# Kernel optimization log

Hardware: AMD Instinct MI355X
Metric: run time of the kernel (lower is better)

The kernel has to match this reference:

```python
import jax, jax.numpy as jnp
import numpy as np

B, N, U = 4096, 128, 128  # batch, num_notes, num_units
F = N - 1                 # per-note feature dim; +1 condition scalar -> LSTM input = N
W_SCALE = 0.08            # ~1/sqrt(U), keeps gates in a sane range


def setup_inputs() -> dict:
    key = jax.random.key(0)
    ks = jax.random.split(key, 12)
    return {
        "note_features": jax.random.normal(ks[0], (B, N, F), jnp.float32),
        "targets": jax.random.uniform(ks[1], (B, N), jnp.float32),
        "w_ih0": jax.random.normal(ks[2], (4 * U, N), jnp.float32) * W_SCALE,
        "w_hh0": jax.random.normal(ks[3], (4 * U, U), jnp.float32) * W_SCALE,
        "b_ih0": jax.random.normal(ks[4], (4 * U,), jnp.float32) * W_SCALE,
        "b_hh0": jax.random.normal(ks[5], (4 * U,), jnp.float32) * W_SCALE,
        "w_ih1": jax.random.normal(ks[6], (4 * U, U), jnp.float32) * W_SCALE,
        "w_hh1": jax.random.normal(ks[7], (4 * U, U), jnp.float32) * W_SCALE,
        "b_ih1": jax.random.normal(ks[8], (4 * U,), jnp.float32) * W_SCALE,
        "b_hh1": jax.random.normal(ks[9], (4 * U,), jnp.float32) * W_SCALE,
        "w_out": jax.random.normal(ks[10], (1, U), jnp.float32) * W_SCALE,
        "b_out": jax.random.normal(ks[11], (1,), jnp.float32) * W_SCALE,
    }


def _lstm_cell(x, h, c, w_ih, w_hh, b_ih, b_hh):
    # PyTorch gate order: i, f, g, o
    gates = x @ w_ih.T + b_ih + h @ w_hh.T + b_hh  # [B, 4U]
    i, f, g, o = jnp.split(gates, 4, axis=-1)
    c_new = jax.nn.sigmoid(f) * c + jax.nn.sigmoid(i) * jnp.tanh(g)
    h_new = jax.nn.sigmoid(o) * jnp.tanh(c_new)
    return h_new, c_new


def reference(note_features, targets, w_ih0, w_hh0, b_ih0, b_hh0,
              w_ih1, w_hh1, b_ih1, b_hh1, w_out, b_out):
    b = note_features.shape[0]
    # teacher-forced condition: previous target note, zero at step 0
    cond = jnp.concatenate([jnp.zeros((b, 1), note_features.dtype), targets[:, :-1]], axis=1)
    x_seq = jnp.concatenate([note_features, cond[..., None]], axis=-1)  # [B, N, N]
    x_seq = jnp.transpose(x_seq, (1, 0, 2))                              # [N, B, N]

    zeros = jnp.zeros((b, U), note_features.dtype)

    def step(carry, x):
        h0, c0, h1, c1 = carry
        h0, c0 = _lstm_cell(x, h0, c0, w_ih0, w_hh0, b_ih0, b_hh0)
        h1, c1 = _lstm_cell(h0, h1, c1, w_ih1, w_hh1, b_ih1, b_hh1)
        return (h0, c0, h1, c1), h1

    _, hs = jax.lax.scan(step, (zeros, zeros, zeros, zeros), x_seq)  # [N, B, U]
    logits = jnp.einsum('nbu,ou->nbo', hs, w_out) + b_out            # [N, B, 1]
    return jnp.transpose(jax.nn.sigmoid(logits)[..., 0], (1, 0))     # [B, N]
```

## Files before the change

kernel.cpp:

```cpp
#include <hip/hip_runtime.h>
#include <math.h>

typedef _Float16 f16;
typedef _Float16 f16x8 __attribute__((ext_vector_type(8)));
typedef float f32x4 __attribute__((ext_vector_type(4)));

#define NSTEP 128
#define FEAT  127
#define BLK_B 16
#define NBLOCK 256
#define NTHREADS 512

__device__ __forceinline__ float sigf(float x) { return 1.0f / (1.0f + __expf(-x)); }
__device__ __forceinline__ float tanh_(float x) { return 1.0f - 2.0f / (1.0f + __expf(2.0f * x)); }

__device__ __forceinline__ void sync_lds() {
    asm volatile("s_waitcnt lgkmcnt(0)" ::: "memory");
    __builtin_amdgcn_s_barrier();
    asm volatile("" ::: "memory");
}

#define PIN(v) asm volatile("" : "+v"(v))

__global__ void prep_weights(const float* __restrict__ w_ih0,
                             const float* __restrict__ w_hh0,
                             const float* __restrict__ w_ih1,
                             const float* __restrict__ w_hh1,
                             f16* __restrict__ ws16)
{
    int idx = blockIdx.x * blockDim.x + threadIdx.x;
    int j    = idx & 7;
    int lane = (idx >> 3) & 63;
    int ks   = (idx >> 9) & 3;
    int gate = (idx >> 11) & 3;
    int wave = (idx >> 13) & 7;
    int sel  = (idx >> 16) & 3;
    int n = gate * 128 + wave * 16 + (lane & 15);
    int k = ks * 32 + (lane >> 4) * 8 + j;
    const float* W = (sel == 0) ? w_ih0 : (sel == 1) ? w_hh0 : (sel == 2) ? w_ih1 : w_hh1;
    ws16[idx] = (f16)W[n * 128 + k];
}

__global__ __launch_bounds__(NTHREADS, 2) void lstm_l0(
    const float* __restrict__ nf,   const float* __restrict__ tgt,
    const float* __restrict__ b_ih0, const float* __restrict__ b_hh0,
    const f16* __restrict__ wfrag,  f16* __restrict__ h0g)
{
    __shared__ __align__(16) f16 xs[2][16][152];
    __shared__ __align__(16) f16 h0s[2][16][152];

    const int tid  = threadIdx.x;
    const int wave = tid >> 6;
    const int lane = tid & 63;
    const int col  = lane & 15;
    const int quad = lane >> 4;
    const int b0   = blockIdx.x * BLK_B;
    const int u    = wave * 16 + col;

    for (int i = tid; i < 2 * 16 * 152; i += NTHREADS)
        (&h0s[0][0][0])[i] = (f16)0.0f;

    float bias0[4];
#pragma unroll
    for (int g = 0; g < 4; ++g)
        bias0[g] = b_ih0[g * 128 + u] + b_hh0[g * 128 + u];

    const f16x8* wf = (const f16x8*)wfrag;

    f16x8 wih0[4][4], whh0[4][4];
#pragma unroll
    for (int g = 0; g < 4; ++g)
#pragma unroll
        for (int ks = 0; ks < 4; ++ks) {
            const int fi = ((wave * 4 + g) * 4 + ks) * 64 + lane;
            wih0[g][ks] = wf[0 * 8192 + fi];
            whh0[g][ks] = wf[1 * 8192 + fi];
            PIN(wih0[g][ks]);
            PIN(whh0[g][ks]);
        }

    const float* px[2][2];
    int pxs[2][2];
#pragma unroll
    for (int rr = 0; rr < 2; ++rr) {
        const long rowg = b0 + wave * 2 + rr;
#pragma unroll
        for (int h = 0; h < 2; ++h) {
            const int k = lane + 64 * h;
            if (k < FEAT) { px[rr][h] = nf + (rowg * NSTEP + 1) * FEAT + k; pxs[rr][h] = FEAT; }
            else          { px[rr][h] = tgt + rowg * NSTEP;                 pxs[rr][h] = 1; }
        }
    }

    f16* hp = h0g + (long)(b0 + quad * 4) * NSTEP * 128 + u;

    f32x4 c0 = {0.f, 0.f, 0.f, 0.f};

#pragma unroll
    for (int rr = 0; rr < 2; ++rr) {
        const int row = wave * 2 + rr;
        const long gbt = (long)(b0 + row) * NSTEP;
#pragma unroll
        for (int h = 0; h < 2; ++h) {
            const int k = lane + 64 * h;
            xs[0][row][k] = (f16)((k < FEAT) ? nf[gbt * FEAT + k] : 0.0f);
        }
    }
    sync_lds();

    for (int t = 0; t < NSTEP; ++t) {
        const int pa = t & 1, wb = pa ^ 1;

        float xnv[2][2] = {{0.f, 0.f}, {0.f, 0.f}};
        if (t + 1 < NSTEP) {
#pragma unroll
            for (int rr = 0; rr < 2; ++rr)
#pragma unroll
                for (int h = 0; h < 2; ++h)
                    xnv[rr][h] = *px[rr][h];
        }

        f16x8 ax[4], ah[4];
#pragma unroll
        for (int ks = 0; ks < 4; ++ks) {
            ax[ks] = *(const f16x8*)&xs[pa][col][ks * 32 + quad * 8];
            ah[ks] = *(const f16x8*)&h0s[pa][col][ks * 32 + quad * 8];
        }

        f32x4 accx[4], acch[4];
#pragma unroll
        for (int g = 0; g < 4; ++g) {
            accx[g] = (f32x4){bias0[g], bias0[g], bias0[g], bias0[g]};
            acch[g] = (f32x4){0.f, 0.f, 0.f, 0.f};
        }
#pragma unroll
        for (int ks = 0; ks < 4; ++ks)
#pragma unroll
            for (int g = 0; g < 4; ++g)
                accx[g] = __builtin_amdgcn_mfma_f32_16x16x32_f16(ax[ks], wih0[g][ks], accx[g], 0, 0, 0);
#pragma unroll
        for (int ks = 0; ks < 4; ++ks)
#pragma unroll
            for (int g = 0; g < 4; ++g)
                acch[g] = __builtin_amdgcn_mfma_f32_16x16x32_f16(ah[ks], whh0[g][ks], acch[g], 0, 0, 0);

        float h0n[4];
#pragma unroll
        for (int r = 0; r < 4; ++r) {
            const float ig = sigf(accx[0][r] + acch[0][r]);
            const float fg = sigf(accx[1][r] + acch[1][r]);
            const float gg = tanh_(accx[2][r] + acch[2][r]);
            const float og = sigf(accx[3][r] + acch[3][r]);
            const float cn = fg * c0[r] + ig * gg;
            c0[r] = cn;
            h0n[r] = og * tanh_(cn);
        }
#pragma unroll
        for (int r = 0; r < 4; ++r) {
            h0s[wb][quad * 4 + r][u] = (f16)h0n[r];
            hp[r * (NSTEP * 128)] = (f16)h0n[r];
        }
        hp += 128;

        if (t + 1 < NSTEP) {
#pragma unroll
            for (int rr = 0; rr < 2; ++rr)
#pragma unroll
                for (int h = 0; h < 2; ++h) {
                    xs[wb][wave * 2 + rr][lane + 64 * h] = (f16)xnv[rr][h];
                    px[rr][h] += pxs[rr][h];
                }
        }
        sync_lds();
    }
}

__global__ __launch_bounds__(NTHREADS, 2) void lstm_l1(
    const f16* __restrict__ h0g,
    const float* __restrict__ b_ih1, const float* __restrict__ b_hh1,
    const float* __restrict__ w_out, const float* __restrict__ b_out,
    const f16* __restrict__ wfrag,  float* __restrict__ out)
{
    __shared__ __align__(16) f16 hx[2][16][152];
    __shared__ __align__(16) f16 h1s[2][16][152];
    __shared__ float outp[2][8][16];

    const int tid  = threadIdx.x;
    const int wave = tid >> 6;
    const int lane = tid & 63;
    const int col  = lane & 15;
    const int quad = lane >> 4;
    const int b0   = blockIdx.x * BLK_B;
    const int u    = wave * 16 + col;

    for (int i = tid; i < 2 * 16 * 152; i += NTHREADS)
        (&h1s[0][0][0])[i] = (f16)0.0f;

    float bias1[4];
#pragma unroll
    for (int g = 0; g < 4; ++g)
        bias1[g] = b_ih1[g * 128 + u] + b_hh1[g * 128 + u];
    const float wo_u = w_out[u];
    const float bout = b_out[0];

    const f16x8* wf = (const f16x8*)wfrag;

    f16x8 wih1[4][4], whh1[4][4];
#pragma unroll
    for (int g = 0; g < 4; ++g)
#pragma unroll
        for (int ks = 0; ks < 4; ++ks) {
            const int fi = ((wave * 4 + g) * 4 + ks) * 64 + lane;
            wih1[g][ks] = wf[2 * 8192 + fi];
            whh1[g][ks] = wf[3 * 8192 + fi];
            PIN(wih1[g][ks]);
            PIN(whh1[g][ks]);
        }

    const unsigned* rp[2];
#pragma unroll
    for (int rr = 0; rr < 2; ++rr) {
        const int row = wave * 2 + rr;
        rp[rr] = (const unsigned*)(h0g + ((long)(b0 + row) * NSTEP + 1) * 128) + lane;
    }

    f32x4 c1 = {0.f, 0.f, 0.f, 0.f};

#pragma unroll
    for (int rr = 0; rr < 2; ++rr) {
        const int row = wave * 2 + rr;
        const unsigned* sp = (const unsigned*)(h0g + ((long)(b0 + row) * NSTEP) * 128);
        *(unsigned*)&hx[0][row][lane * 2] = sp[lane];
    }
    sync_lds();

    for (int t = 0; t < NSTEP; ++t) {
        const int pa = t & 1, wb = pa ^ 1;

        unsigned hnv[2] = {0u, 0u};
        if (t + 1 < NSTEP) {
#pragma unroll
            for (int rr = 0; rr < 2; ++rr)
                hnv[rr] = rp[rr][0];
        }

        f16x8 axv[4], ahv[4];
#pragma unroll
        for (int ks = 0; ks < 4; ++ks) {
            axv[ks] = *(const f16x8*)&hx[pa][col][ks * 32 + quad * 8];
            ahv[ks] = *(const f16x8*)&h1s[pa][col][ks * 32 + quad * 8];
        }

        f32x4 accx[4], acch[4];
#pragma unroll
        for (int g = 0; g < 4; ++g) {
            accx[g] = (f32x4){bias1[g], bias1[g], bias1[g], bias1[g]};
            acch[g] = (f32x4){0.f, 0.f, 0.f, 0.f};
        }
#pragma unroll
        for (int ks = 0; ks < 4; ++ks)
#pragma unroll
            for (int g = 0; g < 4; ++g)
                accx[g] = __builtin_amdgcn_mfma_f32_16x16x32_f16(axv[ks], wih1[g][ks], accx[g], 0, 0, 0);
#pragma unroll
        for (int ks = 0; ks < 4; ++ks)
#pragma unroll
            for (int g = 0; g < 4; ++g)
                acch[g] = __builtin_amdgcn_mfma_f32_16x16x32_f16(ahv[ks], whh1[g][ks], acch[g], 0, 0, 0);

        float h1n[4];
#pragma unroll
        for (int r = 0; r < 4; ++r) {
            const float ig = sigf(accx[0][r] + acch[0][r]);
            const float fg = sigf(accx[1][r] + acch[1][r]);
            const float gg = tanh_(accx[2][r] + acch[2][r]);
            const float og = sigf(accx[3][r] + acch[3][r]);
            const float cn = fg * c1[r] + ig * gg;
            c1[r] = cn;
            h1n[r] = og * tanh_(cn);
        }
#pragma unroll
        for (int r = 0; r < 4; ++r)
            h1s[wb][quad * 4 + r][u] = (f16)h1n[r];

        float ps[4];
#pragma unroll
        for (int r = 0; r < 4; ++r) ps[r] = h1n[r] * wo_u;
#pragma unroll
        for (int m = 1; m < 16; m <<= 1) {
#pragma unroll
            for (int r = 0; r < 4; ++r) ps[r] += __shfl_xor(ps[r], m, 64);
        }
        if (col == 0) {
#pragma unroll
            for (int r = 0; r < 4; ++r) outp[pa][wave][quad * 4 + r] = ps[r];
        }

        if (t + 1 < NSTEP) {
#pragma unroll
            for (int rr = 0; rr < 2; ++rr) {
                *(unsigned*)&hx[wb][wave * 2 + rr][lane * 2] = hnv[rr];
                rp[rr] += 64;
            }
        }

        sync_lds();

        if (tid < 16) {
            float s = bout;
#pragma unroll
            for (int w = 0; w < 8; ++w) s += outp[pa][w][tid];
            out[(long)(b0 + tid) * NSTEP + t] = sigf(s);
        }
    }
}

__global__ __launch_bounds__(NTHREADS, 2) void lstm_fb(
    const float* __restrict__ nf,   const float* __restrict__ tgt,
    const float* __restrict__ b_ih0, const float* __restrict__ b_hh0,
    const float* __restrict__ b_ih1, const float* __restrict__ b_hh1,
    const float* __restrict__ w_out, const float* __restrict__ b_out,
    const f16* __restrict__ wfrag,  float* __restrict__ out)
{
    __shared__ f16 xs[2][16][152];
    __shared__ f16 h0s[2][16][152];
    __shared__ f16 h1s[2][16][152];
    __shared__ float outp[8][16];

    const int tid  = threadIdx.x;
    const int wave = tid >> 6;
    const int lane = tid & 63;
    const int col  = lane & 15;
    const int quad = lane >> 4;
    const int b0   = blockIdx.x * BLK_B;
    const int u    = wave * 16 + col;

    for (int i = tid; i < 2 * 16 * 152; i += NTHREADS) {
        (&h0s[0][0][0])[i] = (f16)0.0f;
        (&h1s[0][0][0])[i] = (f16)0.0f;
    }
    float bias0[4], bias1[4];
#pragma unroll
    for (int g = 0; g < 4; ++g) {
        bias0[g] = b_ih0[g * 128 + u] + b_hh0[g * 128 + u];
        bias1[g] = b_ih1[g * 128 + u] + b_hh1[g * 128 + u];
    }
    const float wo_u = w_out[u];
    const float bout = b_out[0];
    const f16x8* wf = (const f16x8*)wfrag;

    f32x4 c0 = {0.f, 0.f, 0.f, 0.f};
    f32x4 c1 = {0.f, 0.f, 0.f, 0.f};

#pragma unroll
    for (int rr = 0; rr < 2; ++rr) {
        const int row = wave * 2 + rr;
        const long gbt = (long)(b0 + row) * NSTEP;
#pragma unroll
        for (int h = 0; h < 2; ++h) {
            const int k = lane + 64 * h;
            xs[0][row][k] = (f16)((k < FEAT) ? nf[gbt * FEAT + k] : 0.0f);
        }
    }
    __syncthreads();

    for (int t = 0; t < NSTEP; ++t) {
        const int pa = t & 1, wb = pa ^ 1;
        float xnv[2][2];
#pragma unroll
        for (int rr = 0; rr < 2; ++rr) {
            const int row = wave * 2 + rr;
#pragma unroll
            for (int h = 0; h < 2; ++h) {
                const int k = lane + 64 * h;
                float v = 0.0f;
                if (t + 1 < NSTEP) {
                    const long gbt = (long)(b0 + row) * NSTEP + (t + 1);
                    v = (k < FEAT) ? nf[gbt * FEAT + k] : tgt[(long)(b0 + row) * NSTEP + t];
                }
                xnv[rr][h] = v;
            }
        }
        f32x4 acc[4];
#pragma unroll
        for (int g = 0; g < 4; ++g) acc[g] = (f32x4){bias0[g], bias0[g], bias0[g], bias0[g]};
#pragma unroll
        for (int ks = 0; ks < 4; ++ks) {
            f16x8 a = *(const f16x8*)&xs[pa][col][ks * 32 + quad * 8];
#pragma unroll
            for (int g = 0; g < 4; ++g) {
                f16x8 b = wf[((wave * 4 + g) * 4 + ks) * 64 + lane];
                acc[g] = __builtin_amdgcn_mfma_f32_16x16x32_f16(a, b, acc[g], 0, 0, 0);
            }
        }
#pragma unroll
        for (int ks = 0; ks < 4; ++ks) {
            f16x8 a = *(const f16x8*)&h0s[pa][col][ks * 32 + quad * 8];
#pragma unroll
            for (int g = 0; g < 4; ++g) {
                f16x8 b = wf[1 * 8192 + ((wave * 4 + g) * 4 + ks) * 64 + lane];
                acc[g] = __builtin_amdgcn_mfma_f32_16x16x32_f16(a, b, acc[g], 0, 0, 0);
            }
        }
        float h0n[4];
#pragma unroll
        for (int r = 0; r < 4; ++r) {
            const float ig = sigf(acc[0][r]);
            const float fg = sigf(acc[1][r]);
            const float gg = tanh_(acc[2][r]);
            const float og = sigf(acc[3][r]);
            const float cn = fg * c0[r] + ig * gg;
            c0[r] = cn;
            h0n[r] = og * tanh_(cn);
        }
#pragma unroll
        for (int r = 0; r < 4; ++r) h0s[wb][quad * 4 + r][u] = (f16)h0n[r];
        __syncthreads();

#pragma unroll
        for (int g = 0; g < 4; ++g) acc[g] = (f32x4){bias1[g], bias1[g], bias1[g], bias1[g]};
#pragma unroll
        for (int ks = 0; ks < 4; ++ks) {
            f16x8 a = *(const f16x8*)&h0s[wb][col][ks * 32 + quad * 8];
#pragma unroll
            for (int g = 0; g < 4; ++g) {
                f16x8 b = wf[2 * 8192 + ((wave * 4 + g) * 4 + ks) * 64 + lane];
                acc[g] = __builtin_amdgcn_mfma_f32_16x16x32_f16(a, b, acc[g], 0, 0, 0);
            }
        }
#pragma unroll
        for (int ks = 0; ks < 4; ++ks) {
            f16x8 a = *(const f16x8*)&h1s[pa][col][ks * 32 + quad * 8];
#pragma unroll
            for (int g = 0; g < 4; ++g) {
                f16x8 b = wf[3 * 8192 + ((wave * 4 + g) * 4 + ks) * 64 + lane];
                acc[g] = __builtin_amdgcn_mfma_f32_16x16x32_f16(a, b, acc[g], 0, 0, 0);
            }
        }
        float h1n[4];
#pragma unroll
        for (int r = 0; r < 4; ++r) {
            const float ig = sigf(acc[0][r]);
            const float fg = sigf(acc[1][r]);
            const float gg = tanh_(acc[2][r]);
            const float og = sigf(acc[3][r]);
            const float cn = fg * c1[r] + ig * gg;
            c1[r] = cn;
            h1n[r] = og * tanh_(cn);
        }
#pragma unroll
        for (int r = 0; r < 4; ++r) h1s[wb][quad * 4 + r][u] = (f16)h1n[r];
#pragma unroll
        for (int rr = 0; rr < 2; ++rr) {
            const int row = wave * 2 + rr;
#pragma unroll
            for (int h = 0; h < 2; ++h) xs[wb][row][lane + 64 * h] = (f16)xnv[rr][h];
        }
        float ps[4];
#pragma unroll
        for (int r = 0; r < 4; ++r) ps[r] = h1n[r] * wo_u;
#pragma unroll
        for (int m = 1; m < 16; m <<= 1) {
#pragma unroll
            for (int r = 0; r < 4; ++r) ps[r] += __shfl_xor(ps[r], m, 64);
        }
        if (col == 0) {
#pragma unroll
            for (int r = 0; r < 4; ++r) outp[wave][quad * 4 + r] = ps[r];
        }
        __syncthreads();
        if (tid < 16) {
            float s = bout;
#pragma unroll
            for (int w = 0; w < 8; ++w) s += outp[w][tid];
            out[(long)(b0 + tid) * NSTEP + t] = sigf(s);
        }
    }
}

extern "C" void kernel_launch(void* const* d_in, const int* in_sizes, int n_in,
                              void* d_out, int out_size, void* d_ws, size_t ws_size,
                              hipStream_t stream)
{
    const float* nf    = (const float*)d_in[0];
    const float* tgt   = (const float*)d_in[1];
    const float* w_ih0 = (const float*)d_in[2];
    const float* w_hh0 = (const float*)d_in[3];
    const float* b_ih0 = (const float*)d_in[4];
    const float* b_hh0 = (const float*)d_in[5];
    const float* w_ih1 = (const float*)d_in[6];
    const float* w_hh1 = (const float*)d_in[7];
    const float* b_ih1 = (const float*)d_in[8];
    const float* b_hh1 = (const float*)d_in[9];
    const float* w_out = (const float*)d_in[10];
    const float* b_out = (const float*)d_in[11];

    f16*   ws16 = (f16*)d_ws;
    float* out  = (float*)d_out;

    prep_weights<<<1024, 256, 0, stream>>>(w_ih0, w_hh0, w_ih1, w_hh1, ws16);

    const size_t need = 512 * 1024 + (size_t)4096 * 128 * 128 * 2;
    if (ws_size >= need) {
        f16* h0g = ws16 + 4 * 65536;
        lstm_l0<<<NBLOCK, NTHREADS, 0, stream>>>(nf, tgt, b_ih0, b_hh0, ws16, h0g);
        lstm_l1<<<NBLOCK, NTHREADS, 0, stream>>>(h0g, b_ih1, b_hh1, w_out, b_out, ws16, out);
    } else {
        lstm_fb<<<NBLOCK, NTHREADS, 0, stream>>>(nf, tgt, b_ih0, b_hh0, b_ih1, b_hh1,
                                                 w_out, b_out, ws16, out);
    }
}
```

Before: 800.2 us.

## Fuse layer-0 and layer-1 LSTM kernels into one launch, drop weight prep

Merges the two per-layer kernels into a single kernel that runs layer 0 over all steps, then layer 1, in the same block. This removes the separate weight-prep launch and two extra launches by converting fp32 weights to f16 fragments directly in registers. Layer 1 now loads its h0 input fragments straight from global memory into registers, prefetched one step ahead, instead of staging them through LDS. The output-projection reduction uses DPP row operations instead of shuffles, and the first MFMA of each gate starts from the bias vector or zero. The cost is strided fp32 weight loads at startup and an h0 round-trip through global memory inside one kernel, which now relies on the block reading back only what it wrote.

```diff
diff --git a/kernel.cpp b/kernel.cpp
--- a/kernel.cpp
+++ b/kernel.cpp
@@ -21,6 +21,263 @@
 }
 
 #define PIN(v) asm volatile("" : "+v"(v))
+
+__device__ __forceinline__ f16x8 load_wfrag(const float* __restrict__ W, int n, int k) {
+    const float* p = W + n * 128 + k;
+    f16x8 r;
+#pragma unroll
+    for (int j = 0; j < 8; ++j) r[j] = (f16)p[j];
+    return r;
+}
+
+__device__ __forceinline__ float row16_sum(float v) {
+    int t;
+    t = __builtin_amdgcn_update_dpp(0, __float_as_int(v), 0x118, 0xf, 0xf, true);
+    v += __int_as_float(t);
+    t = __builtin_amdgcn_update_dpp(0, __float_as_int(v), 0x114, 0xf, 0xf, true);
+    v += __int_as_float(t);
+    t = __builtin_amdgcn_update_dpp(0, __float_as_int(v), 0x112, 0xf, 0xf, true);
+    v += __int_as_float(t);
+    t = __builtin_amdgcn_update_dpp(0, __float_as_int(v), 0x111, 0xf, 0xf, true);
+    v += __int_as_float(t);
+    return v;
+}
+
+__global__ __launch_bounds__(NTHREADS, 2) void lstm_fused(
+    const float* __restrict__ nf,    const float* __restrict__ tgt,
+    const float* __restrict__ w_ih0, const float* __restrict__ w_hh0,
+    const float* __restrict__ b_ih0, const float* __restrict__ b_hh0,
+    const float* __restrict__ w_ih1, const float* __restrict__ w_hh1,
+    const float* __restrict__ b_ih1, const float* __restrict__ b_hh1,
+    const float* __restrict__ w_out, const float* __restrict__ b_out,
+    f16* __restrict__ h0g, float* __restrict__ out)
+{
+    __shared__ __align__(16) f16 bufA[2][16][152];
+    __shared__ __align__(16) f16 bufB[2][16][152];
+    __shared__ float outp[2][8][16];
+
+    const int tid  = threadIdx.x;
+    const int wave = tid >> 6;
+    const int lane = tid & 63;
+    const int col  = lane & 15;
+    const int quad = lane >> 4;
+    const int b0   = blockIdx.x * BLK_B;
+    const int u    = wave * 16 + col;
+    const f32x4 zz = {0.f, 0.f, 0.f, 0.f};
+
+    {
+        for (int i = tid; i < 2 * 16 * 152; i += NTHREADS)
+            (&bufB[0][0][0])[i] = (f16)0.0f;
+
+        f32x4 bv0[4];
+#pragma unroll
+        for (int g = 0; g < 4; ++g) {
+            const float b = b_ih0[g * 128 + u] + b_hh0[g * 128 + u];
+            bv0[g] = (f32x4){b, b, b, b};
+        }
+
+        f16x8 wih0[4][4], whh0[4][4];
+#pragma unroll
+        for (int g = 0; g < 4; ++g)
+#pragma unroll
+            for (int ks = 0; ks < 4; ++ks) {
+                wih0[g][ks] = load_wfrag(w_ih0, g * 128 + u, ks * 32 + quad * 8);
+                whh0[g][ks] = load_wfrag(w_hh0, g * 128 + u, ks * 32 + quad * 8);
+                PIN(wih0[g][ks]);
+                PIN(whh0[g][ks]);
+            }
+
+        const float* px[2][2];
+        int pxs[2][2];
+#pragma unroll
+        for (int rr = 0; rr < 2; ++rr) {
+            const long rowg = b0 + wave * 2 + rr;
+#pragma unroll
+            for (int h = 0; h < 2; ++h) {
+                const int k = lane + 64 * h;
+                if (k < FEAT) { px[rr][h] = nf + (rowg * NSTEP + 1) * FEAT + k; pxs[rr][h] = FEAT; }
+                else          { px[rr][h] = tgt + rowg * NSTEP;                 pxs[rr][h] = 1; }
+            }
+        }
+
+        f16* hp = h0g + (long)(b0 + quad * 4) * NSTEP * 128 + u;
+
+        f32x4 c0 = {0.f, 0.f, 0.f, 0.f};
+
+#pragma unroll
+        for (int rr = 0; rr < 2; ++rr) {
+            const int row = wave * 2 + rr;
+            const long gbt = (long)(b0 + row) * NSTEP;
+#pragma unroll
+            for (int h = 0; h < 2; ++h) {
+                const int k = lane + 64 * h;
+                bufA[0][row][k] = (f16)((k < FEAT) ? nf[gbt * FEAT + k] : 0.0f);
+            }
+        }
+        sync_lds();
+
+        for (int t = 0; t < NSTEP; ++t) {
+            const int pa = t & 1, wb = pa ^ 1;
+
+            float xnv[2][2] = {{0.f, 0.f}, {0.f, 0.f}};
+            if (t + 1 < NSTEP) {
+#pragma unroll
+                for (int rr = 0; rr < 2; ++rr)
+#pragma unroll
+                    for (int h = 0; h < 2; ++h)
+                        xnv[rr][h] = *px[rr][h];
+            }
+
+            f16x8 ax[4], ah[4];
+#pragma unroll
+            for (int ks = 0; ks < 4; ++ks) {
+                ax[ks] = *(const f16x8*)&bufA[pa][col][ks * 32 + quad * 8];
+                ah[ks] = *(const f16x8*)&bufB[pa][col][ks * 32 + quad * 8];
+            }
+
+            f32x4 accx[4], acch[4];
+#pragma unroll
+            for (int g = 0; g < 4; ++g) {
+                accx[g] = __builtin_amdgcn_mfma_f32_16x16x32_f16(ax[0], wih0[g][0], bv0[g], 0, 0, 0);
+                acch[g] = __builtin_amdgcn_mfma_f32_16x16x32_f16(ah[0], whh0[g][0], zz, 0, 0, 0);
+            }
+#pragma unroll
+            for (int ks = 1; ks < 4; ++ks)
+#pragma unroll
+                for (int g = 0; g < 4; ++g) {
+                    accx[g] = __builtin_amdgcn_mfma_f32_16x16x32_f16(ax[ks], wih0[g][ks], accx[g], 0, 0, 0);
+                    acch[g] = __builtin_amdgcn_mfma_f32_16x16x32_f16(ah[ks], whh0[g][ks], acch[g], 0, 0, 0);
+                }
+
+            float h0n[4];
+#pragma unroll
+            for (int r = 0; r < 4; ++r) {
+                const float ig = sigf(accx[0][r] + acch[0][r]);
+                const float fg = sigf(accx[1][r] + acch[1][r]);
+                const float gg = tanh_(accx[2][r] + acch[2][r]);
+                const float og = sigf(accx[3][r] + acch[3][r]);
+                const float cn = fg * c0[r] + ig * gg;
+                c0[r] = cn;
+                h0n[r] = og * tanh_(cn);
+            }
+#pragma unroll
+            for (int r = 0; r < 4; ++r) {
+                bufB[wb][quad * 4 + r][u] = (f16)h0n[r];
+                hp[r * (NSTEP * 128)] = (f16)h0n[r];
+            }
+            hp += 128;
+
+            if (t + 1 < NSTEP) {
+#pragma unroll
+                for (int rr = 0; rr < 2; ++rr)
+#pragma unroll
+                    for (int h = 0; h < 2; ++h) {
+                        bufA[wb][wave * 2 + rr][lane + 64 * h] = (f16)xnv[rr][h];
+                        px[rr][h] += pxs[rr][h];
+                    }
+            }
+            sync_lds();
+        }
+    }
+
+    __syncthreads();
+    for (int i = tid; i < 2 * 16 * 152; i += NTHREADS)
+        (&bufA[0][0][0])[i] = (f16)0.0f;
+    __syncthreads();
+
+    {
+        f32x4 bv1[4];
+#pragma unroll
+        for (int g = 0; g < 4; ++g) {
+            const float b = b_ih1[g * 128 + u] + b_hh1[g * 128 + u];
+            bv1[g] = (f32x4){b, b, b, b};
+        }
+        const float wo_u = w_out[u];
+        const float bout = b_out[0];
+
+        f16x8 wih1[4][4], whh1[4][4];
+#pragma unroll
+        for (int g = 0; g < 4; ++g)
+#pragma unroll
+            for (int ks = 0; ks < 4; ++ks) {
+                wih1[g][ks] = load_wfrag(w_ih1, g * 128 + u, ks * 32 + quad * 8);
+                whh1[g][ks] = load_wfrag(w_hh1, g * 128 + u, ks * 32 + quad * 8);
+                PIN(wih1[g][ks]);
+                PIN(whh1[g][ks]);
+            }
+
+        f32x4 c1 = {0.f, 0.f, 0.f, 0.f};
+
+        const f16* hrow = h0g + (long)(b0 + col) * NSTEP * 128 + quad * 8;
+        f16x8 nx[4];
+#pragma unroll
+        for (int ks = 0; ks < 4; ++ks)
+            nx[ks] = *(const f16x8*)(hrow + ks * 32);
+        const f16* hnext = hrow + 128;
+
+        for (int t = 0; t < NSTEP; ++t) {
+            const int pa = t & 1, wb = pa ^ 1;
+
+            f16x8 ahv[4];
+#pragma unroll
+            for (int ks = 0; ks < 4; ++ks)
+                ahv[ks] = *(const f16x8*)&bufA[pa][col][ks * 32 + quad * 8];
+
+            f32x4 accx[4], acch[4];
+#pragma unroll
+            for (int g = 0; g < 4; ++g) {
+                accx[g] = __builtin_amdgcn_mfma_f32_16x16x32_f16(nx[0], wih1[g][0], bv1[g], 0, 0, 0);
+                acch[g] = __builtin_amdgcn_mfma_f32_16x16x32_f16(ahv[0], whh1[g][0], zz, 0, 0, 0);
+            }
+#pragma unroll
+            for (int ks = 1; ks < 4; ++ks)
+#pragma unroll
+                for (int g = 0; g < 4; ++g) {
+                    accx[g] = __builtin_amdgcn_mfma_f32_16x16x32_f16(nx[ks], wih1[g][ks], accx[g], 0, 0, 0);
+                    acch[g] = __builtin_amdgcn_mfma_f32_16x16x32_f16(ahv[ks], whh1[g][ks], acch[g], 0, 0, 0);
+                }
+
+            if (t + 1 < NSTEP) {
+#pragma unroll
+                for (int ks = 0; ks < 4; ++ks)
+                    nx[ks] = *(const f16x8*)(hnext + ks * 32);
+                hnext += 128;
+            }
+
+            float h1n[4];
+#pragma unroll
+            for (int r = 0; r < 4; ++r) {
+                const float ig = sigf(accx[0][r] + acch[0][r]);
+                const float fg = sigf(accx[1][r] + acch[1][r]);
+                const float gg = tanh_(accx[2][r] + acch[2][r]);
+                const float og = sigf(accx[3][r] + acch[3][r]);
+                const float cn = fg * c1[r] + ig * gg;
+                c1[r] = cn;
+                h1n[r] = og * tanh_(cn);
+            }
+#pragma unroll
+            for (int r = 0; r < 4; ++r)
+                bufA[wb][quad * 4 + r][u] = (f16)h1n[r];
+
+            float ps[4];
+#pragma unroll
+            for (int r = 0; r < 4; ++r) ps[r] = row16_sum(h1n[r] * wo_u);
+            if (col == 15) {
+#pragma unroll
+                for (int r = 0; r < 4; ++r) outp[pa][wave][quad * 4 + r] = ps[r];
+            }
+
+            sync_lds();
+
+            if (tid < 16) {
+                float s = bout;
+#pragma unroll
+                for (int w = 0; w < 8; ++w) s += outp[pa][w][tid];
+                out[(long)(b0 + tid) * NSTEP + t] = sigf(s);
+            }
+        }
+    }
+}
 
 __global__ void prep_weights(const float* __restrict__ w_ih0,
                              const float* __restrict__ w_hh0,
@@ -41,280 +298,6 @@
     ws16[idx] = (f16)W[n * 128 + k];
 }
 
-__global__ __launch_bounds__(NTHREADS, 2) void lstm_l0(
-    const float* __restrict__ nf,   const float* __restrict__ tgt,
-    const float* __restrict__ b_ih0, const float* __restrict__ b_hh0,
-    const f16* __restrict__ wfrag,  f16* __restrict__ h0g)
-{
-    __shared__ __align__(16) f16 xs[2][16][152];
-    __shared__ __align__(16) f16 h0s[2][16][152];
-
-    const int tid  = threadIdx.x;
-    const int wave = tid >> 6;
-    const int lane = tid & 63;
-    const int col  = lane & 15;
-    const int quad = lane >> 4;
-    const int b0   = blockIdx.x * BLK_B;
-    const int u    = wave * 16 + col;
-
-    for (int i = tid; i < 2 * 16 * 152; i += NTHREADS)
-        (&h0s[0][0][0])[i] = (f16)0.0f;
-
-    float bias0[4];
-#pragma unroll
-    for (int g = 0; g < 4; ++g)
-        bias0[g] = b_ih0[g * 128 + u] + b_hh0[g * 128 + u];
-
-    const f16x8* wf = (const f16x8*)wfrag;
-
-    f16x8 wih0[4][4], whh0[4][4];
-#pragma unroll
-    for (int g = 0; g < 4; ++g)
-#pragma unroll
-        for (int ks = 0; ks < 4; ++ks) {
-            const int fi = ((wave * 4 + g) * 4 + ks) * 64 + lane;
-            wih0[g][ks] = wf[0 * 8192 + fi];
-            whh0[g][ks] = wf[1 * 8192 + fi];
-            PIN(wih0[g][ks]);
-            PIN(whh0[g][ks]);
-        }
-
-    const float* px[2][2];
-    int pxs[2][2];
-#pragma unroll
-    for (int rr = 0; rr < 2; ++rr) {
-        const long rowg = b0 + wave * 2 + rr;
-#pragma unroll
-        for (int h = 0; h < 2; ++h) {
-            const int k = lane + 64 * h;
-            if (k < FEAT) { px[rr][h] = nf + (rowg * NSTEP + 1) * FEAT + k; pxs[rr][h] = FEAT; }
-            else          { px[rr][h] = tgt + rowg * NSTEP;                 pxs[rr][h] = 1; }
-        }
-    }
-
-    f16* hp = h0g + (long)(b0 + quad * 4) * NSTEP * 128 + u;
-
-    f32x4 c0 = {0.f, 0.f, 0.f, 0.f};
-
-#pragma unroll
-    for (int rr = 0; rr < 2; ++rr) {
-        const int row = wave * 2 + rr;
-        const long gbt = (long)(b0 + row) * NSTEP;
-#pragma unroll
-        for (int h = 0; h < 2; ++h) {
-            const int k = lane + 64 * h;
-            xs[0][row][k] = (f16)((k < FEAT) ? nf[gbt * FEAT + k] : 0.0f);
-        }
-    }
-    sync_lds();
-
-    for (int t = 0; t < NSTEP; ++t) {
-        const int pa = t & 1, wb = pa ^ 1;
-
-        float xnv[2][2] = {{0.f, 0.f}, {0.f, 0.f}};
-        if (t + 1 < NSTEP) {
-#pragma unroll
-            for (int rr = 0; rr < 2; ++rr)
-#pragma unroll
-                for (int h = 0; h < 2; ++h)
-                    xnv[rr][h] = *px[rr][h];
-        }
-
-        f16x8 ax[4], ah[4];
-#pragma unroll
-        for (int ks = 0; ks < 4; ++ks) {
-            ax[ks] = *(const f16x8*)&xs[pa][col][ks * 32 + quad * 8];
-            ah[ks] = *(const f16x8*)&h0s[pa][col][ks * 32 + quad * 8];
-        }
-
-        f32x4 accx[4], acch[4];
-#pragma unroll
-        for (int g = 0; g < 4; ++g) {
-            accx[g] = (f32x4){bias0[g], bias0[g], bias0[g], bias0[g]};
-            acch[g] = (f32x4){0.f, 0.f, 0.f, 0.f};
-        }
-#pragma unroll
-        for (int ks = 0; ks < 4; ++ks)
-#pragma unroll
-            for (int g = 0; g < 4; ++g)
-                accx[g] = __builtin_amdgcn_mfma_f32_16x16x32_f16(ax[ks], wih0[g][ks], accx[g], 0, 0, 0);
-#pragma unroll
-        for (int ks = 0; ks < 4; ++ks)
-#pragma unroll
-            for (int g = 0; g < 4; ++g)
-                acch[g] = __builtin_amdgcn_mfma_f32_16x16x32_f16(ah[ks], whh0[g][ks], acch[g], 0, 0, 0);
-
-        float h0n[4];
-#pragma unroll
-        for (int r = 0; r < 4; ++r) {
-            const float ig = sigf(accx[0][r] + acch[0][r]);
-            const float fg = sigf(accx[1][r] + acch[1][r]);
-            const float gg = tanh_(accx[2][r] + acch[2][r]);
-            const float og = sigf(accx[3][r] + acch[3][r]);
-            const float cn = fg * c0[r] + ig * gg;
-            c0[r] = cn;
-            h0n[r] = og * tanh_(cn);
-        }
-#pragma unroll
-        for (int r = 0; r < 4; ++r) {
-            h0s[wb][quad * 4 + r][u] = (f16)h0n[r];
-            hp[r * (NSTEP * 128)] = (f16)h0n[r];
-        }
-        hp += 128;
-
-        if (t + 1 < NSTEP) {
-#pragma unroll
-            for (int rr = 0; rr < 2; ++rr)
-#pragma unroll
-                for (int h = 0; h < 2; ++h) {
-                    xs[wb][wave * 2 + rr][lane + 64 * h] = (f16)xnv[rr][h];
-                    px[rr][h] += pxs[rr][h];
-                }
-        }
-        sync_lds();
-    }
-}
-
-__global__ __launch_bounds__(NTHREADS, 2) void lstm_l1(
-    const f16* __restrict__ h0g,
-    const float* __restrict__ b_ih1, const float* __restrict__ b_hh1,
-    const float* __restrict__ w_out, const float* __restrict__ b_out,
-    const f16* __restrict__ wfrag,  float* __restrict__ out)
-{
-    __shared__ __align__(16) f16 hx[2][16][152];
-    __shared__ __align__(16) f16 h1s[2][16][152];
-    __shared__ float outp[2][8][16];
-
-    const int tid  = threadIdx.x;
-    const int wave = tid >> 6;
-    const int lane = tid & 63;
-    const int col  = lane & 15;
-    const int quad = lane >> 4;
-    const int b0   = blockIdx.x * BLK_B;
-    const int u    = wave * 16 + col;
-
-    for (int i = tid; i < 2 * 16 * 152; i += NTHREADS)
-        (&h1s[0][0][0])[i] = (f16)0.0f;
-
-    float bias1[4];
-#pragma unroll
-    for (int g = 0; g < 4; ++g)
-        bias1[g] = b_ih1[g * 128 + u] + b_hh1[g * 128 + u];
-    const float wo_u = w_out[u];
-    const float bout = b_out[0];
-
-    const f16x8* wf = (const f16x8*)wfrag;
-
-    f16x8 wih1[4][4], whh1[4][4];
-#pragma unroll
-    for (int g = 0; g < 4; ++g)
-#pragma unroll
-        for (int ks = 0; ks < 4; ++ks) {
-            const int fi = ((wave * 4 + g) * 4 + ks) * 64 + lane;
-            wih1[g][ks] = wf[2 * 8192 + fi];
-            whh1[g][ks] = wf[3 * 8192 + fi];
-            PIN(wih1[g][ks]);
-            PIN(whh1[g][ks]);
-        }
-
-    const unsigned* rp[2];
-#pragma unroll
-    for (int rr = 0; rr < 2; ++rr) {
-        const int row = wave * 2 + rr;
-        rp[rr] = (const unsigned*)(h0g + ((long)(b0 + row) * NSTEP + 1) * 128) + lane;
-    }
-
-    f32x4 c1 = {0.f, 0.f, 0.f, 0.f};
-
-#pragma unroll
-    for (int rr = 0; rr < 2; ++rr) {
-        const int row = wave * 2 + rr;
-        const unsigned* sp = (const unsigned*)(h0g + ((long)(b0 + row) * NSTEP) * 128);
-        *(unsigned*)&hx[0][row][lane * 2] = sp[lane];
-    }
-    sync_lds();
-
-    for (int t = 0; t < NSTEP; ++t) {
-        const int pa = t & 1, wb = pa ^ 1;
-
-        unsigned hnv[2] = {0u, 0u};
-        if (t + 1 < NSTEP) {
-#pragma unroll
-            for (int rr = 0; rr < 2; ++rr)
-                hnv[rr] = rp[rr][0];
-        }
-
-        f16x8 axv[4], ahv[4];
-#pragma unroll
-        for (int ks = 0; ks < 4; ++ks) {
-            axv[ks] = *(const f16x8*)&hx[pa][col][ks * 32 + quad * 8];
-            ahv[ks] = *(const f16x8*)&h1s[pa][col][ks * 32 + quad * 8];
-        }
-
-        f32x4 accx[4], acch[4];
-#pragma unroll
-        for (int g = 0; g < 4; ++g) {
-            accx[g] = (f32x4){bias1[g], bias1[g], bias1[g], bias1[g]};
-            acch[g] = (f32x4){0.f, 0.f, 0.f, 0.f};
-        }
-#pragma unroll
-        for (int ks = 0; ks < 4; ++ks)
-#pragma unroll
-            for (int g = 0; g < 4; ++g)
-                accx[g] = __builtin_amdgcn_mfma_f32_16x16x32_f16(axv[ks], wih1[g][ks], accx[g], 0, 0, 0);
-#pragma unroll
-        for (int ks = 0; ks < 4; ++ks)
-#pragma unroll
-            for (int g = 0; g < 4; ++g)
-                acch[g] = __builtin_amdgcn_mfma_f32_16x16x32_f16(ahv[ks], whh1[g][ks], acch[g], 0, 0, 0);
-
-        float h1n[4];
-#pragma unroll
-        for (int r = 0; r < 4; ++r) {
-            const float ig = sigf(accx[0][r] + acch[0][r]);
-            const float fg = sigf(accx[1][r] + acch[1][r]);
-            const float gg = tanh_(accx[2][r] + acch[2][r]);
-            const float og = sigf(accx[3][r] + acch[3][r]);
-            const float cn = fg * c1[r] + ig * gg;
-            c1[r] = cn;
-            h1n[r] = og * tanh_(cn);
-        }
-#pragma unroll
-        for (int r = 0; r < 4; ++r)
-            h1s[wb][quad * 4 + r][u] = (f16)h1n[r];
-
-        float ps[4];
-#pragma unroll
-        for (int r = 0; r < 4; ++r) ps[r] = h1n[r] * wo_u;
-#pragma unroll
-        for (int m = 1; m < 16; m <<= 1) {
-#pragma unroll
-            for (int r = 0; r < 4; ++r) ps[r] += __shfl_xor(ps[r], m, 64);
-        }
-        if (col == 0) {
-#pragma unroll
-            for (int r = 0; r < 4; ++r) outp[pa][wave][quad * 4 + r] = ps[r];
-        }
-
-        if (t + 1 < NSTEP) {
-#pragma unroll
-            for (int rr = 0; rr < 2; ++rr) {
-                *(unsigned*)&hx[wb][wave * 2 + rr][lane * 2] = hnv[rr];
-                rp[rr] += 64;
-            }
-        }
-
-        sync_lds();
-
-        if (tid < 16) {
-            float s = bout;
-#pragma unroll
-            for (int w = 0; w < 8; ++w) s += outp[pa][w][tid];
-            out[(long)(b0 + tid) * NSTEP + t] = sigf(s);
-        }
-    }
-}
-
 __global__ __launch_bounds__(NTHREADS, 2) void lstm_fb(
     const float* __restrict__ nf,   const float* __restrict__ tgt,
     const float* __restrict__ b_ih0, const float* __restrict__ b_hh0,
@@ -495,17 +478,17 @@
     const float* w_out = (const float*)d_in[10];
     const float* b_out = (const float*)d_in[11];
 
-    f16*   ws16 = (f16*)d_ws;
-    float* out  = (float*)d_out;
-
-    prep_weights<<<1024, 256, 0, stream>>>(w_ih0, w_hh0, w_ih1, w_hh1, ws16);
-
-    const size_t need = 512 * 1024 + (size_t)4096 * 128 * 128 * 2;
+    float* out = (float*)d_out;
+
+    const size_t need = (size_t)4096 * 128 * 128 * 2;
     if (ws_size >= need) {
-        f16* h0g = ws16 + 4 * 65536;
-        lstm_l0<<<NBLOCK, NTHREADS, 0, stream>>>(nf, tgt, b_ih0, b_hh0, ws16, h0g);
-        lstm_l1<<<NBLOCK, NTHREADS, 0, stream>>>(h0g, b_ih1, b_hh1, w_out, b_out, ws16, out);
+        f16* h0g = (f16*)d_ws;
+        lstm_fused<<<NBLOCK, NTHREADS, 0, stream>>>(
+            nf, tgt, w_ih0, w_hh0, b_ih0, b_hh0,
+            w_ih1, w_hh1, b_ih1, b_hh1, w_out, b_out, h0g, out);
     } else {
+        f16* ws16 = (f16*)d_ws;
+        prep_weights<<<1024, 256, 0, stream>>>(w_ih0, w_hh0, w_ih1, w_hh1, ws16);
         lstm_fb<<<NBLOCK, NTHREADS, 0, stream>>>(nf, tgt, b_ih0, b_hh0, b_ih1, b_hh1,
                                                  w_out, b_out, ws16, out);
     }
```

Measured after the change: 789.9 us. About the same (-1.3%).
